# Kernel tuning notes

Measured on AMD Instinct MI355X. Metric: run time of the kernel, lower is better.

The kernel has to match this reference:

```python
import jax, jax.numpy as jnp
import numpy as np

N_NODES = 100000
N_EDGES = 1600000
D_IN = 128
D_OUT = 128


def setup_inputs() -> dict:
    key = jax.random.key(0)
    k1, k2, k3, k4, k5 = jax.random.split(key, 5)
    h = jax.random.normal(k1, (N_NODES, D_IN), dtype=jnp.float32)
    src = jax.random.randint(k2, (N_EDGES,), 0, N_NODES, dtype=jnp.int64)
    dst = jax.random.randint(k3, (N_EDGES,), 0, N_NODES, dtype=jnp.int64)
    # Glorot-ish init for linear weights (PyTorch nn.Linear style: [out, in])
    scale = 1.0 / np.sqrt(D_IN)
    W_self = jax.random.uniform(k4, (D_OUT, D_IN), jnp.float32, -scale, scale)
    W_neigh = jax.random.uniform(k5, (D_OUT, D_IN), jnp.float32, -scale, scale)
    b = jnp.zeros((D_OUT,), dtype=jnp.float32)
    return {"h": h, "src": src, "dst": dst, "W_self": W_self,
            "W_neigh": W_neigh, "b": b}


def reference(h, src, dst, W_self, W_neigh, b):
    n_nodes = h.shape[0]
    # neighbor gather + segment-mean over in-neighbors (DGL fn.copy_u + fn.mean)
    msg = h[src]                                            # [E, D_in]
    neigh_sum = jax.ops.segment_sum(msg, dst, num_segments=n_nodes)
    deg = jax.ops.segment_sum(jnp.ones_like(dst, dtype=h.dtype), dst,
                              num_segments=n_nodes)         # [N]
    h_neigh = neigh_sum / jnp.maximum(deg, 1.0)[:, None]    # mean; 0 for isolated
    # SAGEConv mean: fc_self(h) + fc_neigh(h_neigh) + bias
    out = h @ W_self.T + h_neigh @ W_neigh.T + b
    return out
```

## Files before the change

kernel.cpp:

```cpp
#include <hip/hip_runtime.h>
#include <stdint.h>

#define NN 100000
#define NE 1600000
#define DD 128
#define NTILES ((NN + 127) / 128)
#define NB 256
#define CHUNK (NE / NB)
#define NBUCK ((NN + 255) / 256)
#define GH_N (NBUCK * NB)
#define GH_BLK (GH_N / 256)

typedef __bf16 bf16x8 __attribute__((ext_vector_type(8)));
typedef float f32x4 __attribute__((ext_vector_type(4)));
typedef float f32x2 __attribute__((ext_vector_type(2)));

__device__ __forceinline__ unsigned int f2bf2(float a, float b) {
  union { float f; unsigned u; } x, y;
  x.f = a; y.f = b;
  unsigned ua = x.u + (0x7FFFu + ((x.u >> 16) & 1u));
  unsigned ub = y.u + (0x7FFFu + ((y.u >> 16) & 1u));
  return (ua >> 16) | (ub & 0xFFFF0000u);
}

__global__ __launch_bounds__(256) void convert_h8_kernel(const float4* __restrict__ hp,
                                                         uint2* __restrict__ h8) {
  int gid = blockIdx.x * 256 + threadIdx.x;
  float4 a = hp[2 * gid], b = hp[2 * gid + 1];
  int lo = __builtin_amdgcn_cvt_pk_fp8_f32(a.x, a.y, 0, false);
  lo = __builtin_amdgcn_cvt_pk_fp8_f32(a.z, a.w, lo, true);
  int hi = __builtin_amdgcn_cvt_pk_fp8_f32(b.x, b.y, 0, false);
  hi = __builtin_amdgcn_cvt_pk_fp8_f32(b.z, b.w, hi, true);
  h8[gid] = make_uint2((unsigned)lo, (unsigned)hi);
}

__global__ __launch_bounds__(256) void coarse_hist_kernel(const int* __restrict__ dst,
                                                          int* __restrict__ gh) {
  __shared__ int lh[NBUCK];
  int t = threadIdx.x, b = blockIdx.x;
  for (int i = t; i < NBUCK; i += 256) lh[i] = 0;
  __syncthreads();
  int e0 = b * CHUNK;
  for (int e = e0 + t; e < e0 + CHUNK; e += 256)
    atomicAdd(&lh[dst[e] >> 8], 1);
  __syncthreads();
  for (int i = t; i < NBUCK; i += 256) gh[i * NB + b] = lh[i];
}

__global__ __launch_bounds__(256) void blocksum_kernel(const int* __restrict__ gh,
                                                       int* __restrict__ bsum) {
  __shared__ int s[256];
  int t = threadIdx.x;
  s[t] = gh[blockIdx.x * 256 + t];
  __syncthreads();
  for (int d = 128; d > 0; d >>= 1) {
    if (t < d) s[t] += s[t + d];
    __syncthreads();
  }
  if (t == 0) bsum[blockIdx.x] = s[0];
}

__global__ __launch_bounds__(512) void scanbsum_kernel(const int* __restrict__ bsum,
                                                       int* __restrict__ bsum_ex) {
  __shared__ int s[512];
  int t = threadIdx.x;
  int v = (t < GH_BLK) ? bsum[t] : 0;
  s[t] = v;
  __syncthreads();
  for (int d = 1; d < 512; d <<= 1) {
    int x = (t >= d) ? s[t - d] : 0;
    __syncthreads();
    s[t] += x;
    __syncthreads();
  }
  if (t < GH_BLK) bsum_ex[t] = s[t] - v;
}

__global__ __launch_bounds__(256) void scanfull_kernel(const int* __restrict__ gh,
                                                       const int* __restrict__ bsum_ex,
                                                       int* __restrict__ gsc) {
  __shared__ int s[256];
  int t = threadIdx.x;
  int idx = blockIdx.x * 256 + t;
  int v = gh[idx];
  s[t] = v;
  __syncthreads();
  for (int d = 1; d < 256; d <<= 1) {
    int x = (t >= d) ? s[t - d] : 0;
    __syncthreads();
    s[t] += x;
    __syncthreads();
  }
  gsc[idx] = bsum_ex[blockIdx.x] + s[t] - v;
}

__global__ __launch_bounds__(256) void coarse_scatter_kernel(
    const int* __restrict__ src, const int* __restrict__ dst,
    const int* __restrict__ gsc, unsigned* __restrict__ ebuf) {
  __shared__ int lhpad[512];
  __shared__ int lbase[NBUCK];
  __shared__ int lcur[NBUCK];
  __shared__ int gstart[NBUCK];
  __shared__ unsigned sdata[CHUNK];
  __shared__ int sgpos[CHUNK];
  int t = threadIdx.x, b = blockIdx.x;
  lhpad[t] = 0;
  lhpad[t + 256] = 0;
  __syncthreads();
  int e0 = b * CHUNK;
  for (int e = e0 + t; e < e0 + CHUNK; e += 256)
    atomicAdd(&lhpad[dst[e] >> 8], 1);
  __syncthreads();
  int cnt0 = lhpad[t], cnt1 = lhpad[t + 256];
  for (int d = 1; d < 512; d <<= 1) {
    int x0 = (t >= d) ? lhpad[t - d] : 0;
    int x1 = ((t + 256) >= d) ? lhpad[t + 256 - d] : 0;
    __syncthreads();
    lhpad[t] += x0;
    lhpad[t + 256] += x1;
    __syncthreads();
  }
  if (t < NBUCK) { lbase[t] = lhpad[t] - cnt0; lcur[t] = 0; gstart[t] = gsc[t * NB + b]; }
  int i2 = t + 256;
  if (i2 < NBUCK) { lbase[i2] = lhpad[i2] - cnt1; lcur[i2] = 0; gstart[i2] = gsc[i2 * NB + b]; }
  __syncthreads();
  for (int e = e0 + t; e < e0 + CHUNK; e += 256) {
    int d = dst[e], s = src[e];
    int bk = d >> 8;
    int slot = atomicAdd(&lcur[bk], 1);
    int lp = lbase[bk] + slot;
    sdata[lp] = ((unsigned)(d & 255) << 24) | (unsigned)s;
    sgpos[lp] = gstart[bk] + slot;
  }
  __syncthreads();
  for (int j = t; j < CHUNK; j += 256) ebuf[sgpos[j]] = sdata[j];
}

__global__ __launch_bounds__(256) void fine_sort_kernel(const unsigned* __restrict__ ebuf,
                                                        const int* __restrict__ gsc,
                                                        int* __restrict__ csr,
                                                        int* __restrict__ offs) {
  __shared__ int hist[256], scn[256], cur[256];
  int t = threadIdx.x, g = blockIdx.x;
  int base = gsc[g * NB];
  int end = (g == NBUCK - 1) ? NE : gsc[(g + 1) * NB];
  hist[t] = 0;
  __syncthreads();
  for (int j = base + t; j < end; j += 256)
    atomicAdd(&hist[ebuf[j] >> 24], 1);
  __syncthreads();
  int v = hist[t];
  scn[t] = v;
  __syncthreads();
  for (int d = 1; d < 256; d <<= 1) {
    int x = (t >= d) ? scn[t - d] : 0;
    __syncthreads();
    scn[t] += x;
    __syncthreads();
  }
  int excl = scn[t] - v;
  int node = g * 256 + t;
  if (node < NN) offs[node] = base + excl;
  if (node == NN - 1) offs[NN] = NE;
  cur[t] = excl;
  __syncthreads();
  for (int j = base + t; j < end; j += 256) {
    unsigned p = ebuf[j];
    int pos = atomicAdd(&cur[p >> 24], 1);
    csr[base + pos] = (int)(p & 0x00FFFFFFu);
  }
}

__device__ __forceinline__ void acc16(float* a, uint4 u) {
  f32x2 p;
  p = __builtin_amdgcn_cvt_pk_f32_fp8(u.x, false); a[0] += p.x;  a[1] += p.y;
  p = __builtin_amdgcn_cvt_pk_f32_fp8(u.x, true);  a[2] += p.x;  a[3] += p.y;
  p = __builtin_amdgcn_cvt_pk_f32_fp8(u.y, false); a[4] += p.x;  a[5] += p.y;
  p = __builtin_amdgcn_cvt_pk_f32_fp8(u.y, true);  a[6] += p.x;  a[7] += p.y;
  p = __builtin_amdgcn_cvt_pk_f32_fp8(u.z, false); a[8] += p.x;  a[9] += p.y;
  p = __builtin_amdgcn_cvt_pk_f32_fp8(u.z, true);  a[10] += p.x; a[11] += p.y;
  p = __builtin_amdgcn_cvt_pk_f32_fp8(u.w, false); a[12] += p.x; a[13] += p.y;
  p = __builtin_amdgcn_cvt_pk_f32_fp8(u.w, true);  a[14] += p.x; a[15] += p.y;
}

__global__ __launch_bounds__(256) void gather_kernel(const uint4* __restrict__ h8,
                                                     const int* __restrict__ offs,
                                                     const int* __restrict__ csr,
                                                     uint4* __restrict__ hneighbf4) {
  int q = (blockIdx.x * 256 + threadIdx.x) >> 3;
  int l = threadIdx.x & 7;
  if (q >= NN) return;
  int off0 = offs[q], off1 = offs[q + 1];
  float a[16];
#pragma unroll
  for (int i = 0; i < 16; i++) a[i] = 0.f;
  int j = off0;
  for (; j + 4 <= off1; j += 4) {
    int s0 = csr[j], s1 = csr[j + 1], s2 = csr[j + 2], s3 = csr[j + 3];
    uint4 u0 = h8[(size_t)s0 * 8 + l];
    uint4 u1 = h8[(size_t)s1 * 8 + l];
    uint4 u2 = h8[(size_t)s2 * 8 + l];
    uint4 u3 = h8[(size_t)s3 * 8 + l];
    acc16(a, u0); acc16(a, u1); acc16(a, u2); acc16(a, u3);
  }
  for (; j < off1; j++) acc16(a, h8[(size_t)csr[j] * 8 + l]);
  int deg = off1 - off0;
  float sc = (deg > 0) ? (1.0f / (float)deg) : 0.0f;
  uint4 r0, r1;
  r0.x = f2bf2(a[0] * sc, a[1] * sc);   r0.y = f2bf2(a[2] * sc, a[3] * sc);
  r0.z = f2bf2(a[4] * sc, a[5] * sc);   r0.w = f2bf2(a[6] * sc, a[7] * sc);
  r1.x = f2bf2(a[8] * sc, a[9] * sc);   r1.y = f2bf2(a[10] * sc, a[11] * sc);
  r1.z = f2bf2(a[12] * sc, a[13] * sc); r1.w = f2bf2(a[14] * sc, a[15] * sc);
  hneighbf4[(size_t)q * 16 + 2 * l] = r0;
  hneighbf4[(size_t)q * 16 + 2 * l + 1] = r1;
}

__device__ __forceinline__ void stage_f32(const float* __restrict__ X,
                                          int row0, int nvalid,
                                          uint4* buf, int t) {
#pragma unroll
  for (int i = 0; i < 8; i++) {
    int id = t + (i << 8);
    int r = id >> 4;
    int c8 = id & 15;
    int row = row0 + r;
    float4 v0 = {0.f, 0.f, 0.f, 0.f}, v1 = {0.f, 0.f, 0.f, 0.f};
    if (row < nvalid) {
      const float4* p = (const float4*)(X + (size_t)row * DD + (c8 << 3));
      v0 = p[0];
      v1 = p[1];
    }
    uint4 q;
    q.x = f2bf2(v0.x, v0.y);
    q.y = f2bf2(v0.z, v0.w);
    q.z = f2bf2(v1.x, v1.y);
    q.w = f2bf2(v1.z, v1.w);
    int rt = r >> 4, m = r & 15, kc = c8 >> 2, quad = c8 & 3;
    buf[(((rt << 2) + kc) << 6) + (quad << 4) + m] = q;
  }
}

__device__ __forceinline__ void stage_bf(const uint4* __restrict__ X,
                                         int row0, int nvalid,
                                         uint4* buf, int t) {
#pragma unroll
  for (int i = 0; i < 8; i++) {
    int d = t + (i << 8);
    int rt = d >> 8, kc = (d >> 6) & 3, quad = (d >> 4) & 3, m = d & 15;
    int r = rt * 16 + m, c8 = kc * 4 + quad;
    int row = row0 + r;
    uint4 q = {0u, 0u, 0u, 0u};
    if (row < nvalid) q = X[(size_t)row * 16 + c8];
    buf[d] = q;
  }
}

__device__ __forceinline__ void compute_half(const uint4* sA, const uint4* sW,
                                             f32x4 acc[2][8], int wv, int lane) {
#pragma unroll
  for (int kc = 0; kc < 4; kc++) {
    bf16x8 b[8];
#pragma unroll
    for (int n = 0; n < 8; n++)
      b[n] = *(const bf16x8*)&sW[(((n << 2) + kc) << 6) + lane];
    bf16x8 a0 = *(const bf16x8*)&sA[((((wv * 2 + 0) << 2) + kc) << 6) + lane];
    bf16x8 a1 = *(const bf16x8*)&sA[((((wv * 2 + 1) << 2) + kc) << 6) + lane];
#pragma unroll
    for (int n = 0; n < 8; n++) {
      acc[0][n] = __builtin_amdgcn_mfma_f32_16x16x32_bf16(a0, b[n], acc[0][n], 0, 0, 0);
      acc[1][n] = __builtin_amdgcn_mfma_f32_16x16x32_bf16(a1, b[n], acc[1][n], 0, 0, 0);
    }
  }
}

__global__ __launch_bounds__(256) void gemm_kernel(
    const float* __restrict__ h, const uint4* __restrict__ hneighbf,
    const float* __restrict__ Wself, const float* __restrict__ Wneigh,
    const float* __restrict__ bias, float* __restrict__ out) {
  __shared__ uint4 sA[2048];
  __shared__ uint4 sW[2048];
  int t = threadIdx.x;
  int wv = t >> 6;
  int lane = t & 63;
  int row0 = blockIdx.x * 128;

  f32x4 acc[2][8];
#pragma unroll
  for (int i = 0; i < 2; i++)
#pragma unroll
    for (int n = 0; n < 8; n++) acc[i][n] = f32x4{0.f, 0.f, 0.f, 0.f};

  stage_f32(h, row0, NN, sA, t);
  stage_f32(Wself, 0, 128, sW, t);
  __syncthreads();
  compute_half(sA, sW, acc, wv, lane);
  __syncthreads();

  stage_bf(hneighbf, row0, NN, sA, t);
  stage_f32(Wneigh, 0, 128, sW, t);
  __syncthreads();
  compute_half(sA, sW, acc, wv, lane);

  int col = lane & 15, rq = lane >> 4;
  float bv[8];
#pragma unroll
  for (int n = 0; n < 8; n++) bv[n] = bias[n * 16 + col];
#pragma unroll
  for (int rt = 0; rt < 2; rt++) {
    int rb = row0 + (wv * 2 + rt) * 16 + rq * 4;
#pragma unroll
    for (int r = 0; r < 4; r++) {
      int row = rb + r;
      if (row < NN) {
        float* op = out + (size_t)row * DD + col;
#pragma unroll
        for (int n = 0; n < 8; n++) op[n * 16] = acc[rt][n][r] + bv[n];
      }
    }
  }
}

extern "C" void kernel_launch(void* const* d_in, const int* in_sizes, int n_in,
                              void* d_out, int out_size, void* d_ws, size_t ws_size,
                              hipStream_t stream) {
  const float* h      = (const float*)d_in[0];
  const int*   src    = (const int*)d_in[1];
  const int*   dst    = (const int*)d_in[2];
  const float* Wself  = (const float*)d_in[3];
  const float* Wneigh = (const float*)d_in[4];
  const float* bias   = (const float*)d_in[5];
  float* out = (float*)d_out;

  char* ws = (char*)d_ws;
  unsigned* h8       = (unsigned*)ws;
  unsigned* hneighbf = (unsigned*)(ws + 12800000);
  unsigned* ebuf     = (unsigned*)(ws + 12800000);
  int*      csr      = (int*)(ws + 38400000);
  int*      gh       = (int*)(ws + 44800000);
  int*      gsc      = (int*)(ws + 45200384);
  int*      bsum     = (int*)(ws + 45600768);
  int*      bsum_ex  = (int*)(ws + 45602336);
  int*      offs     = (int*)(ws + 45603904);

  convert_h8_kernel<<<6250, 256, 0, stream>>>((const float4*)h, (uint2*)h8);
  coarse_hist_kernel<<<NB, 256, 0, stream>>>(dst, gh);
  blocksum_kernel<<<GH_BLK, 256, 0, stream>>>(gh, bsum);
  scanbsum_kernel<<<1, 512, 0, stream>>>(bsum, bsum_ex);
  scanfull_kernel<<<GH_BLK, 256, 0, stream>>>(gh, bsum_ex, gsc);
  coarse_scatter_kernel<<<NB, 256, 0, stream>>>(src, dst, gsc, ebuf);
  fine_sort_kernel<<<NBUCK, 256, 0, stream>>>(ebuf, gsc, csr, offs);
  gather_kernel<<<(NN * 8 + 255) / 256, 256, 0, stream>>>(
      (const uint4*)h8, offs, csr, (uint4*)hneighbf);
  gemm_kernel<<<NTILES, 256, 0, stream>>>(h, (const uint4*)hneighbf,
                                          Wself, Wneigh, bias, out);
}
```

Before: 226.7 us.

## Fuse neighbor mean gather into GEMM kernel and use packed f32x2 accumulation

The separate gather kernel is removed. Each GEMM block now gathers and averages the fp8 neighbor rows for its own 128 nodes and writes the bf16 results straight into shared memory before the W_neigh half of the matmul. This avoids writing the intermediate h_neigh buffer to global memory, reading it back, and one kernel launch. Accumulation uses packed f32x2 adds. The gather now runs with far fewer threads in flight, since 782 large-LDS blocks each handle 4 nodes per thread sequentially, so latency hiding for the random loads may suffer.

Result: slower. 240.2 us (+6.0%).

```diff
diff --git a/kernel.cpp b/kernel.cpp
--- a/kernel.cpp
+++ b/kernel.cpp
@@ -171,48 +171,15 @@
   }
 }
 
-__device__ __forceinline__ void acc16(float* a, uint4 u) {
-  f32x2 p;
-  p = __builtin_amdgcn_cvt_pk_f32_fp8(u.x, false); a[0] += p.x;  a[1] += p.y;
-  p = __builtin_amdgcn_cvt_pk_f32_fp8(u.x, true);  a[2] += p.x;  a[3] += p.y;
-  p = __builtin_amdgcn_cvt_pk_f32_fp8(u.y, false); a[4] += p.x;  a[5] += p.y;
-  p = __builtin_amdgcn_cvt_pk_f32_fp8(u.y, true);  a[6] += p.x;  a[7] += p.y;
-  p = __builtin_amdgcn_cvt_pk_f32_fp8(u.z, false); a[8] += p.x;  a[9] += p.y;
-  p = __builtin_amdgcn_cvt_pk_f32_fp8(u.z, true);  a[10] += p.x; a[11] += p.y;
-  p = __builtin_amdgcn_cvt_pk_f32_fp8(u.w, false); a[12] += p.x; a[13] += p.y;
-  p = __builtin_amdgcn_cvt_pk_f32_fp8(u.w, true);  a[14] += p.x; a[15] += p.y;
-}
-
-__global__ __launch_bounds__(256) void gather_kernel(const uint4* __restrict__ h8,
-                                                     const int* __restrict__ offs,
-                                                     const int* __restrict__ csr,
-                                                     uint4* __restrict__ hneighbf4) {
-  int q = (blockIdx.x * 256 + threadIdx.x) >> 3;
-  int l = threadIdx.x & 7;
-  if (q >= NN) return;
-  int off0 = offs[q], off1 = offs[q + 1];
-  float a[16];
-#pragma unroll
-  for (int i = 0; i < 16; i++) a[i] = 0.f;
-  int j = off0;
-  for (; j + 4 <= off1; j += 4) {
-    int s0 = csr[j], s1 = csr[j + 1], s2 = csr[j + 2], s3 = csr[j + 3];
-    uint4 u0 = h8[(size_t)s0 * 8 + l];
-    uint4 u1 = h8[(size_t)s1 * 8 + l];
-    uint4 u2 = h8[(size_t)s2 * 8 + l];
-    uint4 u3 = h8[(size_t)s3 * 8 + l];
-    acc16(a, u0); acc16(a, u1); acc16(a, u2); acc16(a, u3);
-  }
-  for (; j < off1; j++) acc16(a, h8[(size_t)csr[j] * 8 + l]);
-  int deg = off1 - off0;
-  float sc = (deg > 0) ? (1.0f / (float)deg) : 0.0f;
-  uint4 r0, r1;
-  r0.x = f2bf2(a[0] * sc, a[1] * sc);   r0.y = f2bf2(a[2] * sc, a[3] * sc);
-  r0.z = f2bf2(a[4] * sc, a[5] * sc);   r0.w = f2bf2(a[6] * sc, a[7] * sc);
-  r1.x = f2bf2(a[8] * sc, a[9] * sc);   r1.y = f2bf2(a[10] * sc, a[11] * sc);
-  r1.z = f2bf2(a[12] * sc, a[13] * sc); r1.w = f2bf2(a[14] * sc, a[15] * sc);
-  hneighbf4[(size_t)q * 16 + 2 * l] = r0;
-  hneighbf4[(size_t)q * 16 + 2 * l + 1] = r1;
+__device__ __forceinline__ void acc16p(f32x2* a, uint4 u) {
+  a[0] += __builtin_amdgcn_cvt_pk_f32_fp8(u.x, false);
+  a[1] += __builtin_amdgcn_cvt_pk_f32_fp8(u.x, true);
+  a[2] += __builtin_amdgcn_cvt_pk_f32_fp8(u.y, false);
+  a[3] += __builtin_amdgcn_cvt_pk_f32_fp8(u.y, true);
+  a[4] += __builtin_amdgcn_cvt_pk_f32_fp8(u.z, false);
+  a[5] += __builtin_amdgcn_cvt_pk_f32_fp8(u.z, true);
+  a[6] += __builtin_amdgcn_cvt_pk_f32_fp8(u.w, false);
+  a[7] += __builtin_amdgcn_cvt_pk_f32_fp8(u.w, true);
 }
 
 __device__ __forceinline__ void stage_f32(const float* __restrict__ X,
@@ -240,21 +207,6 @@
   }
 }
 
-__device__ __forceinline__ void stage_bf(const uint4* __restrict__ X,
-                                         int row0, int nvalid,
-                                         uint4* buf, int t) {
-#pragma unroll
-  for (int i = 0; i < 8; i++) {
-    int d = t + (i << 8);
-    int rt = d >> 8, kc = (d >> 6) & 3, quad = (d >> 4) & 3, m = d & 15;
-    int r = rt * 16 + m, c8 = kc * 4 + quad;
-    int row = row0 + r;
-    uint4 q = {0u, 0u, 0u, 0u};
-    if (row < nvalid) q = X[(size_t)row * 16 + c8];
-    buf[d] = q;
-  }
-}
-
 __device__ __forceinline__ void compute_half(const uint4* sA, const uint4* sW,
                                              f32x4 acc[2][8], int wv, int lane) {
 #pragma unroll
@@ -273,8 +225,9 @@
   }
 }
 
-__global__ __launch_bounds__(256) void gemm_kernel(
-    const float* __restrict__ h, const uint4* __restrict__ hneighbf,
+__global__ __launch_bounds__(256) void fused_gemm_kernel(
+    const float* __restrict__ h, const uint4* __restrict__ h8,
+    const int* __restrict__ offs, const int* __restrict__ csr,
     const float* __restrict__ Wself, const float* __restrict__ Wneigh,
     const float* __restrict__ bias, float* __restrict__ out) {
   __shared__ uint4 sA[2048];
@@ -284,20 +237,58 @@
   int lane = t & 63;
   int row0 = blockIdx.x * 128;
 
+  stage_f32(Wneigh, 0, 128, sW, t);
+
+  int nsub = t >> 3;
+  int l = t & 7;
+#pragma unroll
+  for (int p = 0; p < 4; p++) {
+    int r = p * 32 + nsub;
+    int q = row0 + r;
+    int off0 = 0, off1 = 0;
+    if (q < NN) { off0 = offs[q]; off1 = offs[q + 1]; }
+    f32x2 a[8];
+#pragma unroll
+    for (int i = 0; i < 8; i++) a[i] = f32x2{0.f, 0.f};
+    int j = off0;
+    for (; j + 4 <= off1; j += 4) {
+      int s0 = csr[j], s1 = csr[j + 1], s2 = csr[j + 2], s3 = csr[j + 3];
+      uint4 u0 = h8[(size_t)s0 * 8 + l];
+      uint4 u1 = h8[(size_t)s1 * 8 + l];
+      uint4 u2 = h8[(size_t)s2 * 8 + l];
+      uint4 u3 = h8[(size_t)s3 * 8 + l];
+      acc16p(a, u0); acc16p(a, u1); acc16p(a, u2); acc16p(a, u3);
+    }
+    for (; j < off1; j++) acc16p(a, h8[(size_t)csr[j] * 8 + l]);
+    int deg = off1 - off0;
+    float sc = (deg > 0) ? (1.0f / (float)deg) : 0.0f;
+    uint4 r0, r1;
+    r0.x = f2bf2(a[0].x * sc, a[0].y * sc);
+    r0.y = f2bf2(a[1].x * sc, a[1].y * sc);
+    r0.z = f2bf2(a[2].x * sc, a[2].y * sc);
+    r0.w = f2bf2(a[3].x * sc, a[3].y * sc);
+    r1.x = f2bf2(a[4].x * sc, a[4].y * sc);
+    r1.y = f2bf2(a[5].x * sc, a[5].y * sc);
+    r1.z = f2bf2(a[6].x * sc, a[6].y * sc);
+    r1.w = f2bf2(a[7].x * sc, a[7].y * sc);
+    int rt = r >> 4, m = r & 15;
+    int c80 = 2 * l, c81 = 2 * l + 1;
+    sA[(((rt << 2) + (c80 >> 2)) << 6) + ((c80 & 3) << 4) + m] = r0;
+    sA[(((rt << 2) + (c81 >> 2)) << 6) + ((c81 & 3) << 4) + m] = r1;
+  }
+  __syncthreads();
+
   f32x4 acc[2][8];
 #pragma unroll
   for (int i = 0; i < 2; i++)
 #pragma unroll
     for (int n = 0; n < 8; n++) acc[i][n] = f32x4{0.f, 0.f, 0.f, 0.f};
+
+  compute_half(sA, sW, acc, wv, lane);
+  __syncthreads();
 
   stage_f32(h, row0, NN, sA, t);
   stage_f32(Wself, 0, 128, sW, t);
-  __syncthreads();
-  compute_half(sA, sW, acc, wv, lane);
-  __syncthreads();
-
-  stage_bf(hneighbf, row0, NN, sA, t);
-  stage_f32(Wneigh, 0, 128, sW, t);
   __syncthreads();
   compute_half(sA, sW, acc, wv, lane);
 
@@ -333,14 +324,13 @@
 
   char* ws = (char*)d_ws;
   unsigned* h8       = (unsigned*)ws;
-  unsigned* hneighbf = (unsigned*)(ws + 12800000);
   unsigned* ebuf     = (unsigned*)(ws + 12800000);
-  int*      csr      = (int*)(ws + 38400000);
-  int*      gh       = (int*)(ws + 44800000);
-  int*      gsc      = (int*)(ws + 45200384);
-  int*      bsum     = (int*)(ws + 45600768);
-  int*      bsum_ex  = (int*)(ws + 45602336);
-  int*      offs     = (int*)(ws + 45603904);
+  int*      csr      = (int*)(ws + 19200000);
+  int*      gh       = (int*)(ws + 25600000);
+  int*      gsc      = (int*)(ws + 26000384);
+  int*      bsum     = (int*)(ws + 26400768);
+  int*      bsum_ex  = (int*)(ws + 26402336);
+  int*      offs     = (int*)(ws + 26403904);
 
   convert_h8_kernel<<<6250, 256, 0, stream>>>((const float4*)h, (uint2*)h8);
   coarse_hist_kernel<<<NB, 256, 0, stream>>>(dst, gh);
@@ -349,8 +339,6 @@
   scanfull_kernel<<<GH_BLK, 256, 0, stream>>>(gh, bsum_ex, gsc);
   coarse_scatter_kernel<<<NB, 256, 0, stream>>>(src, dst, gsc, ebuf);
   fine_sort_kernel<<<NBUCK, 256, 0, stream>>>(ebuf, gsc, csr, offs);
-  gather_kernel<<<(NN * 8 + 255) / 256, 256, 0, stream>>>(
-      (const uint4*)h8, offs, csr, (uint4*)hneighbf);
-  gemm_kernel<<<NTILES, 256, 0, stream>>>(h, (const uint4*)hneighbf,
-                                          Wself, Wneigh, bias, out);
-}
+  fused_gemm_kernel<<<NTILES, 256, 0, stream>>>(h, (const uint4*)h8, offs, csr,
+                                                Wself, Wneigh, bias, out);
+}
```
